# Performance work log

Hardware: AMD Instinct MI355X
Metric: run time of the kernel (lower is better)

Reference implementation:

```python
import jax, jax.numpy as jnp
import numpy as np

N_NODES = 50000
N_EDGES = 800000
N_GRAPHS = 64
NEG_SLOPE = 0.2  # PyG GATConv default LeakyReLU slope


def _gat_layer(x, src, dst, W, a_src, a_dst, bias, n_nodes):
    """Single-head GATConv: gather -> segment-softmax over dst -> scatter-add."""
    h = x @ W                                   # [N, F]
    e = jax.nn.leaky_relu(
        (h @ a_src)[src] + (h @ a_dst)[dst], NEG_SLOPE)  # [E]
    # numerically-stable segment softmax over incoming edges of each dst node
    m = jax.ops.segment_max(e, dst, num_segments=n_nodes)   # [N]
    e = jnp.exp(e - m[dst])
    s = jax.ops.segment_sum(e, dst, num_segments=n_nodes)   # [N]
    alpha = e / s[dst]                                       # [E]
    out = jax.ops.segment_sum(alpha[:, None] * h[src], dst, num_segments=n_nodes)
    return out + bias


def setup_inputs() -> dict:
    key = jax.random.key(0)
    ks = jax.random.split(key, 16)
    x = jax.random.normal(ks[0], (N_NODES, 3), dtype=jnp.float32)
    edge_index = jax.random.randint(ks[1], (2, N_EDGES), 0, N_NODES, dtype=jnp.int64)
    edge_attr = jax.random.normal(ks[2], (N_EDGES, 4), dtype=jnp.float32)
    batch = jnp.sort(jax.random.randint(ks[3], (N_NODES,), 0, N_GRAPHS, dtype=jnp.int64))

    def glorot(k, shape):
        lim = float(np.sqrt(6.0 / (shape[0] + shape[-1])))
        return jax.random.uniform(k, shape, jnp.float32, -lim, lim)

    return {
        "x": x, "edge_index": edge_index, "edge_attr": edge_attr, "batch": batch,
        "W1": glorot(ks[4], (3, 8)),
        "a_src1": glorot(ks[5], (8,)),
        "a_dst1": glorot(ks[6], (8,)),
        "b1": jnp.zeros((8,), jnp.float32),
        "W2": glorot(ks[7], (8, 256)),
        "a_src2": glorot(ks[8], (256,)),
        "a_dst2": glorot(ks[9], (256,)),
        "b2": jnp.zeros((256,), jnp.float32),
        "fc_w": glorot(ks[10], (256, 1)),
        "fc_b": jnp.zeros((1,), jnp.float32),
    }


def reference(x, edge_index, edge_attr, batch,
              W1, a_src1, a_dst1, b1, W2, a_src2, a_dst2, b2, fc_w, fc_b):
    n = x.shape[0]
    loops = jnp.arange(n, dtype=edge_index.dtype)
    src = jnp.concatenate([edge_index[0], loops])  # add_self_loops=True
    dst = jnp.concatenate([edge_index[1], loops])
    # edge_attr is unused by GATConv when edge_dim=None (PyG default)
    h = jax.nn.relu(_gat_layer(x, src, dst, W1, a_src1, a_dst1, b1, n))
    h = jax.nn.relu(_gat_layer(h, src, dst, W2, a_src2, a_dst2, b2, n))
    h = h @ fc_w + fc_b                               # [N, 1]
    out = jax.ops.segment_sum(h, batch, num_segments=N_GRAPHS)  # global_add_pool
    return out
```

## Files before the change

### kernel.cpp

```cpp
#include <hip/hip_runtime.h>
#include <math.h>

static constexpr int NN = 50000;
static constexpr int NE = 800000;
static constexpr int NG = 64;
static constexpr int CAP = 64;
static constexpr float SLOPE = 0.2f;
static constexpr int WDER_BLK = 3125;

__global__ void __launch_bounds__(256) k_init_all(
    const float* __restrict__ x, const float* __restrict__ W1,
    const float* __restrict__ a1s, const float* __restrict__ a1d,
    const int* __restrict__ ei,
    const float* __restrict__ W2, const float* __restrict__ a2s,
    const float* __restrict__ a2d,
    float* __restrict__ h1, float* __restrict__ hs1, float* __restrict__ hd1,
    int* __restrict__ counts, unsigned short* __restrict__ ell,
    float* __restrict__ w2sd, float* __restrict__ out) {
  if (blockIdx.x == WDER_BLK) {
    if (threadIdx.x < NG) out[threadIdx.x] = 0.f;
    int w = threadIdx.x >> 6, lane = threadIdx.x & 63;
    for (int tt = w * 4; tt < w * 4 + 4; ++tt) {
      int k = tt >> 1, sel = tt & 1;
      const float* a = sel ? a2d : a2s;
      float acc = 0.f;
      for (int j = lane; j < 256; j += 64) acc += W2[256 * k + j] * a[j];
      for (int off = 32; off; off >>= 1) acc += __shfl_down(acc, off);
      if (lane == 0) w2sd[tt] = acc;
    }
    return;
  }
  int t = blockIdx.x * 256 + threadIdx.x;
  if (t < NN) {
    float x0 = x[3*t], x1 = x[3*t+1], x2 = x[3*t+2];
    float hs = 0.f, hd = 0.f;
    float v[8];
#pragma unroll
    for (int f = 0; f < 8; ++f) {
      v[f] = x0 * W1[f] + x1 * W1[8+f] + x2 * W1[16+f];
      hs += v[f] * a1s[f];
      hd += v[f] * a1d[f];
    }
    float4* h4 = reinterpret_cast<float4*>(h1 + 8*t);
    h4[0] = make_float4(v[0], v[1], v[2], v[3]);
    h4[1] = make_float4(v[4], v[5], v[6], v[7]);
    hs1[t] = hs; hd1[t] = hd;
  }
  if (t < NE) {
    int s = ei[t];
    int d = ei[NE + t];
    int r = atomicAdd(&counts[d], 1);
    if (r < CAP) ell[d * CAP + r] = (unsigned short)s;
  }
}

__device__ __forceinline__ void gather16(int n, int l, int deg,
                                         const unsigned short* __restrict__ row,
                                         const float* __restrict__ hs,
                                         const float* __restrict__ hd,
                                         const float* __restrict__ feat,
                                         float acc[8]) {
  float hdn = hd[n];
  float s = 0.f;
#pragma unroll
  for (int f = 0; f < 8; ++f) acc[f] = 0.f;
  for (int j = l - 1; j < deg; j += 16) {
    int src = (j < 0) ? n : (int)row[j];
    float el = hs[src] + hdn;
    el = el >= 0.f ? el : SLOPE * el;
    float w = __expf(el);
    s += w;
    const float4* f4 = reinterpret_cast<const float4*>(feat + 8*src);
    float4 lo = f4[0], hi = f4[1];
    acc[0] += w*lo.x; acc[1] += w*lo.y; acc[2] += w*lo.z; acc[3] += w*lo.w;
    acc[4] += w*hi.x; acc[5] += w*hi.y; acc[6] += w*hi.z; acc[7] += w*hi.w;
  }
#pragma unroll
  for (int off = 8; off; off >>= 1) {
    s += __shfl_xor(s, off, 16);
#pragma unroll
    for (int f = 0; f < 8; ++f) acc[f] += __shfl_xor(acc[f], off, 16);
  }
  float inv = 1.f / s;
#pragma unroll
  for (int f = 0; f < 8; ++f) acc[f] *= inv;
}

__global__ void __launch_bounds__(256) k_layer1(
    const int* __restrict__ counts, const unsigned short* __restrict__ ell,
    const float* __restrict__ h1, const float* __restrict__ hs1,
    const float* __restrict__ hd1, const float* __restrict__ b1,
    const float* __restrict__ w2sd,
    float* __restrict__ out1, float* __restrict__ hs2, float* __restrict__ hd2) {
  int t = blockIdx.x * 256 + threadIdx.x;
  int n = t >> 4, l = t & 15;
  if (n >= NN) return;
  int deg = min(counts[n], CAP);
  float acc[8];
  gather16(n, l, deg, ell + n * CAP, hs1, hd1, h1, acc);
  if (l == 0) {
    float hs = 0.f, hd = 0.f;
    float v[8];
#pragma unroll
    for (int f = 0; f < 8; ++f) {
      v[f] = fmaxf(acc[f] + b1[f], 0.f);
      hs += v[f] * w2sd[2*f];
      hd += v[f] * w2sd[2*f+1];
    }
    float4* o4 = reinterpret_cast<float4*>(out1 + 8*n);
    o4[0] = make_float4(v[0], v[1], v[2], v[3]);
    o4[1] = make_float4(v[4], v[5], v[6], v[7]);
    hs2[n] = hs; hd2[n] = hd;
  }
}

__global__ void __launch_bounds__(256) k_layer2final(
    const int* __restrict__ counts, const unsigned short* __restrict__ ell,
    const float* __restrict__ out1, const float* __restrict__ hs2,
    const float* __restrict__ hd2, const float* __restrict__ b2,
    const float* __restrict__ W2, const float* __restrict__ fcw,
    const float* __restrict__ fcb, const int* __restrict__ batch,
    float* __restrict__ out) {
  __shared__ float sW2[2048];
  __shared__ float sb2[256];
  __shared__ float sfc[256];
  __shared__ float bins[NG];
  for (int i = threadIdx.x; i < 2048; i += 256) sW2[i] = W2[i];
  sb2[threadIdx.x] = b2[threadIdx.x];
  sfc[threadIdx.x] = fcw[threadIdx.x];
  if (threadIdx.x < NG) bins[threadIdx.x] = 0.f;
  __syncthreads();

  int t = blockIdx.x * 256 + threadIdx.x;
  int n = t >> 4, l = t & 15;
  if (n < NN) {
    int deg = min(counts[n], CAP);
    float acc[8];
    gather16(n, l, deg, ell + n * CAP, hs2, hd2, out1, acc);
    float y = 0.f;
    for (int i = 0; i < 16; ++i) {
      int j = l + 16 * i;
      float o = sb2[j];
#pragma unroll
      for (int k = 0; k < 8; ++k) o += acc[k] * sW2[256*k + j];
      o = fmaxf(o, 0.f);
      y += o * sfc[j];
    }
#pragma unroll
    for (int off = 8; off; off >>= 1) y += __shfl_xor(y, off, 16);
    if (l == 0) atomicAdd(&bins[batch[n]], y + fcb[0]);
  }
  __syncthreads();
  if (threadIdx.x < NG) {
    float v = bins[threadIdx.x];
    if (v != 0.f) atomicAdd(&out[threadIdx.x], v);
  }
}

extern "C" void kernel_launch(void* const* d_in, const int* in_sizes, int n_in,
                              void* d_out, int out_size, void* d_ws, size_t ws_size,
                              hipStream_t stream) {
  const float* x    = (const float*)d_in[0];
  const int*   ei   = (const int*)d_in[1];
  const int*   batch= (const int*)d_in[3];
  const float* W1   = (const float*)d_in[4];
  const float* a1s  = (const float*)d_in[5];
  const float* a1d  = (const float*)d_in[6];
  const float* b1   = (const float*)d_in[7];
  const float* W2   = (const float*)d_in[8];
  const float* a2s  = (const float*)d_in[9];
  const float* a2d  = (const float*)d_in[10];
  const float* b2   = (const float*)d_in[11];
  const float* fcw  = (const float*)d_in[12];
  const float* fcb  = (const float*)d_in[13];
  float* out = (float*)d_out;

  float* ws   = (float*)d_ws;
  float* h1   = ws;
  float* out1 = h1   + 400000;
  float* hs1  = out1 + 400000;
  float* hd1  = hs1  + 50000;
  float* hs2  = hd1  + 50000;
  float* hd2  = hs2  + 50000;
  float* w2sd = hd2  + 50000;
  int* counts = (int*)(w2sd + 16);
  unsigned short* ell = (unsigned short*)(counts + 50000);

  hipMemsetAsync(counts, 0, NN * sizeof(int), stream);

  k_init_all<<<3126, 256, 0, stream>>>(x, W1, a1s, a1d, ei, W2, a2s, a2d,
                                       h1, hs1, hd1, counts, ell, w2sd, out);
  k_layer1<<<3125, 256, 0, stream>>>(counts, ell, h1, hs1, hd1, b1, w2sd,
                                     out1, hs2, hd2);
  k_layer2final<<<3125, 256, 0, stream>>>(counts, ell, out1, hs2, hd2, b2,
                                          W2, fcw, fcb, batch, out);
}
```

Before: 188.8 us.

## Build adjacency via atomicExch linked lists and vectorize layer-2 shared-memory weight reads

Edge bucketing now pushes each edge onto a per-destination linked list with atomicExch. A new per-node kernel walks each list to fill the ELL rows and counts, replacing the atomicAdd-based slot assignment. Separately, the layer-2 projection stores W2, b2 and fc weights in shared memory as padded float4 rows, so each lane reads float4 values without bank conflicts. The list walk is a serial pointer chase of about 16 dependent random loads per node and adds a kernel launch, which may cost more than the atomic contention it removes.

```diff
diff --git a/kernel.cpp b/kernel.cpp
--- a/kernel.cpp
+++ b/kernel.cpp
@@ -8,14 +8,14 @@
 static constexpr float SLOPE = 0.2f;
 static constexpr int WDER_BLK = 3125;
 
-__global__ void __launch_bounds__(256) k_init_all(
+__global__ void __launch_bounds__(256) k_init_ll(
     const float* __restrict__ x, const float* __restrict__ W1,
     const float* __restrict__ a1s, const float* __restrict__ a1d,
     const int* __restrict__ ei,
     const float* __restrict__ W2, const float* __restrict__ a2s,
     const float* __restrict__ a2d,
     float* __restrict__ h1, float* __restrict__ hs1, float* __restrict__ hd1,
-    int* __restrict__ counts, unsigned short* __restrict__ ell,
+    int* __restrict__ head, int* __restrict__ next,
     float* __restrict__ w2sd, float* __restrict__ out) {
   if (blockIdx.x == WDER_BLK) {
     if (threadIdx.x < NG) out[threadIdx.x] = 0.f;
@@ -47,11 +47,27 @@
     hs1[t] = hs; hd1[t] = hd;
   }
   if (t < NE) {
-    int s = ei[t];
     int d = ei[NE + t];
-    int r = atomicAdd(&counts[d], 1);
-    if (r < CAP) ell[d * CAP + r] = (unsigned short)s;
-  }
+    int old = atomicExch(&head[d], t);
+    next[t] = old;
+  }
+}
+
+__global__ void __launch_bounds__(256) k_ll2ell(
+    const int* __restrict__ ei, const int* __restrict__ head,
+    const int* __restrict__ next,
+    unsigned short* __restrict__ ell, int* __restrict__ counts) {
+  int n = blockIdx.x * 256 + threadIdx.x;
+  if (n >= NN) return;
+  int e = head[n];
+  int r = 0;
+  unsigned short* row = ell + n * CAP;
+  while (e >= 0) {
+    if (r < CAP) row[r] = (unsigned short)ei[e];
+    ++r;
+    e = next[e];
+  }
+  counts[n] = min(r, CAP);
 }
 
 __device__ __forceinline__ void gather16(int n, int l, int deg,
@@ -95,7 +111,7 @@
   int t = blockIdx.x * 256 + threadIdx.x;
   int n = t >> 4, l = t & 15;
   if (n >= NN) return;
-  int deg = min(counts[n], CAP);
+  int deg = counts[n];
   float acc[8];
   gather16(n, l, deg, ell + n * CAP, hs1, hd1, h1, acc);
   if (l == 0) {
@@ -121,30 +137,42 @@
     const float* __restrict__ W2, const float* __restrict__ fcw,
     const float* __restrict__ fcb, const int* __restrict__ batch,
     float* __restrict__ out) {
-  __shared__ float sW2[2048];
-  __shared__ float sb2[256];
-  __shared__ float sfc[256];
+  __shared__ float4 sW2p[8 * 16 * 17];
+  __shared__ float4 sb2p[16 * 17];
+  __shared__ float4 sfcp[16 * 17];
   __shared__ float bins[NG];
-  for (int i = threadIdx.x; i < 2048; i += 256) sW2[i] = W2[i];
-  sb2[threadIdx.x] = b2[threadIdx.x];
-  sfc[threadIdx.x] = fcw[threadIdx.x];
+  {
+    int j = threadIdx.x;
+    int lw = j >> 4, mw = (j >> 2) & 3, cw = j & 3;
+    int pidx = lw * 17 + mw;
+    reinterpret_cast<float*>(&sb2p[pidx])[cw] = b2[j];
+    reinterpret_cast<float*>(&sfcp[pidx])[cw] = fcw[j];
+#pragma unroll
+    for (int k = 0; k < 8; ++k)
+      reinterpret_cast<float*>(&sW2p[(k * 16 + lw) * 17 + mw])[cw] = W2[k * 256 + j];
+  }
   if (threadIdx.x < NG) bins[threadIdx.x] = 0.f;
   __syncthreads();
 
   int t = blockIdx.x * 256 + threadIdx.x;
   int n = t >> 4, l = t & 15;
   if (n < NN) {
-    int deg = min(counts[n], CAP);
+    int deg = counts[n];
     float acc[8];
     gather16(n, l, deg, ell + n * CAP, hs2, hd2, out1, acc);
     float y = 0.f;
-    for (int i = 0; i < 16; ++i) {
-      int j = l + 16 * i;
-      float o = sb2[j];
-#pragma unroll
-      for (int k = 0; k < 8; ++k) o += acc[k] * sW2[256*k + j];
-      o = fmaxf(o, 0.f);
-      y += o * sfc[j];
+#pragma unroll
+    for (int m = 0; m < 4; ++m) {
+      float4 o = sb2p[l * 17 + m];
+#pragma unroll
+      for (int k = 0; k < 8; ++k) {
+        float4 w = sW2p[(k * 16 + l) * 17 + m];
+        o.x += acc[k] * w.x; o.y += acc[k] * w.y;
+        o.z += acc[k] * w.z; o.w += acc[k] * w.w;
+      }
+      float4 f = sfcp[l * 17 + m];
+      y += fmaxf(o.x, 0.f) * f.x + fmaxf(o.y, 0.f) * f.y +
+           fmaxf(o.z, 0.f) * f.z + fmaxf(o.w, 0.f) * f.w;
     }
 #pragma unroll
     for (int off = 8; off; off >>= 1) y += __shfl_xor(y, off, 16);
@@ -184,12 +212,15 @@
   float* hd2  = hs2  + 50000;
   float* w2sd = hd2  + 50000;
   int* counts = (int*)(w2sd + 16);
-  unsigned short* ell = (unsigned short*)(counts + 50000);
-
-  hipMemsetAsync(counts, 0, NN * sizeof(int), stream);
-
-  k_init_all<<<3126, 256, 0, stream>>>(x, W1, a1s, a1d, ei, W2, a2s, a2d,
-                                       h1, hs1, hd1, counts, ell, w2sd, out);
+  int* head   = counts + 50000;
+  int* next   = head + 50000;
+  unsigned short* ell = (unsigned short*)(next + 800000);
+
+  hipMemsetAsync(head, 0xFF, NN * sizeof(int), stream);
+
+  k_init_ll<<<3126, 256, 0, stream>>>(x, W1, a1s, a1d, ei, W2, a2s, a2d,
+                                      h1, hs1, hd1, head, next, w2sd, out);
+  k_ll2ell<<<(NN + 255) / 256, 256, 0, stream>>>(ei, head, next, ell, counts);
   k_layer1<<<3125, 256, 0, stream>>>(counts, ell, h1, hs1, hd1, b1, w2sd,
                                      out1, hs2, hd2);
   k_layer2final<<<3125, 256, 0, stream>>>(counts, ell, out1, hs2, hd2, b2,
```

New measurement: 198.3 us. 1.05x slower.
